# Performance work log

Hardware: AMD Instinct MI355X
Metric: run time of the kernel (lower is better)

Reference implementation:

```python
import jax, jax.numpy as jnp
import numpy as np

ALPHA = 1000.0  # softmin temperature from the original module


def setup_inputs() -> dict:
    key = jax.random.key(0)
    ks = jax.random.split(key, 10)
    B, D, H, E, K = 8192, 784, 256, 32, 512
    s = 0.05  # small init scale to keep activations/distances numerically sane
    return {
        "x": jax.random.normal(ks[0], (B, D), jnp.float32),
        "cluster_reps": jax.random.normal(ks[1], (K, E), jnp.float32),
        "W1": jax.random.normal(ks[2], (D, H), jnp.float32) * s,
        "b1": jnp.zeros((H,), jnp.float32),
        "W2": jax.random.normal(ks[3], (H, E), jnp.float32) * s,
        "b2": jnp.zeros((E,), jnp.float32),
        "W3": jax.random.normal(ks[4], (E, H), jnp.float32) * s,
        "b3": jnp.zeros((H,), jnp.float32),
        "W4": jax.random.normal(ks[5], (H, D), jnp.float32) * s,
        "b4": jnp.zeros((D,), jnp.float32),
    }


def reference(x, cluster_reps, W1, b1, W2, b2, W3, b3, W4, b4):
    # --- autoencoder: 2-layer MLP encoder / decoder ---
    h = jax.nn.relu(x @ W1 + b1)            # [B, H]
    embeddings = h @ W2 + b2                # [B, E]
    h2 = jax.nn.relu(embeddings @ W3 + b3)  # [B, H]
    reconstruction = h2 @ W4 + b4           # [B, D]

    # --- squared distances to cluster reps: [B, K] ---
    diff = embeddings[:, None, :] - cluster_reps[None, :, :]  # [B, K, E]
    distances = jnp.sum(diff * diff, axis=2)                  # [B, K]

    # --- stable softmin-weighted distances ---
    min_dist = jnp.min(distances, axis=1, keepdims=True)       # [B, 1]
    exponentials = jnp.exp(-ALPHA * (distances - min_dist))    # [B, K]
    sum_exponentials = jnp.sum(exponentials, axis=1, keepdims=True)
    weighted_dists = distances * (exponentials / sum_exponentials)

    return (weighted_dists, distances, reconstruction, embeddings)
```

## Files before the change

kernel.cpp:

```cpp
#include <hip/hip_runtime.h>
#include <cstddef>

#define NB 8192
#define ND 784
#define NH 256
#define NE 32
#define NK 512
#define ALPHA_F 1000.0f

typedef _Float16 h8 __attribute__((ext_vector_type(8)));
typedef float f32x4 __attribute__((ext_vector_type(4)));

#define TW1 25
#define TN1 8
#define NBW1 200
#define TW4 8
#define TN4 25
#define NBW4 200
#define NBW2 8
#define NBW3 8

__global__ __launch_bounds__(256)
void prep4_kernel(const float* __restrict__ W1, _Float16* __restrict__ w1thi,
                  _Float16* __restrict__ w1tlo,
                  const float* __restrict__ W4, _Float16* __restrict__ w4thi,
                  _Float16* __restrict__ w4tlo,
                  const float* __restrict__ W2, _Float16* __restrict__ w2thi,
                  _Float16* __restrict__ w2tlo,
                  const float* __restrict__ W3, _Float16* __restrict__ w3thi,
                  _Float16* __restrict__ w3tlo) {
    __shared__ float tile[32][33];
    const int b   = blockIdx.x;
    const int tid = threadIdx.x;

    const float* W; _Float16 *hi, *lo; int K, N, kt, nt;
    if (b < NBW1) {
        W = W1; hi = w1thi; lo = w1tlo; K = ND; N = NH;
        kt = b % TW1; nt = b / TW1;
    } else if (b < NBW1 + NBW4) {
        const int bb = b - NBW1;
        W = W4; hi = w4thi; lo = w4tlo; K = NH; N = ND;
        kt = bb % TW4; nt = bb / TW4;
    } else if (b < NBW1 + NBW4 + NBW2) {
        W = W2; hi = w2thi; lo = w2tlo; K = NH; N = NE;
        kt = b - (NBW1 + NBW4); nt = 0;
    } else {
        W = W3; hi = w3thi; lo = w3tlo; K = NE; N = NH;
        kt = 0; nt = b - (NBW1 + NBW4 + NBW2);
    }
    const int k0 = kt * 32, n0 = nt * 32;
    const int row = tid >> 3, c4 = (tid & 7) * 4;
    #pragma unroll
    for (int j = 0; j < 4; ++j) {
        const int k = k0 + row, n = n0 + c4 + j;
        tile[row][c4 + j] = (k < K && n < N) ? W[(size_t)k * N + n] : 0.f;
    }
    __syncthreads();
    const int n = n0 + row;
    if (n < N) {
        #pragma unroll
        for (int j = 0; j < 4; ++j) {
            const int k = k0 + c4 + j;
            if (k < K) {
                float w = tile[c4 + j][row];
                _Float16 hh = (_Float16)w;
                float r = w - (float)hh;
                hi[(size_t)n * K + k] = hh;
                lo[(size_t)n * K + k] = (_Float16)(r * 2048.0f);
            }
        }
    }
}

__global__ __launch_bounds__(1024, 4)
void mega_kernel(const float* __restrict__ x, const float* __restrict__ reps,
                 const _Float16* __restrict__ w1thi, const _Float16* __restrict__ w1tlo,
                 const _Float16* __restrict__ w2thi, const _Float16* __restrict__ w2tlo,
                 const _Float16* __restrict__ w3thi, const _Float16* __restrict__ w3tlo,
                 const _Float16* __restrict__ w4thi, const _Float16* __restrict__ w4tlo,
                 const float* __restrict__ b1, const float* __restrict__ b2,
                 const float* __restrict__ b3, const float* __restrict__ b4,
                 float* __restrict__ emb_g, float* __restrict__ recon_g,
                 float* __restrict__ dist_g, float* __restrict__ wout_g) {
    __shared__ __align__(16) unsigned char lds[116480];
    _Float16* R0h  = (_Float16*)lds;
    _Float16* sA   = (_Float16*)(lds + 66560);
    _Float16* hP   = (_Float16*)(lds + 74752);
    float*    es   = (float*)(lds + 107520);
    _Float16* eP   = (_Float16*)(lds + 112128);
    float*    rmin = (float*)(lds + 116224);
    float*    rinv = (float*)(lds + 116352);

    const int tid  = threadIdx.x;
    const int lane = tid & 63;
    const int wv   = tid >> 6;
    const int li   = lane & 15;
    const int kq   = (lane >> 4) * 8;
    const int quad = lane >> 4;
    const int r0   = blockIdx.x * 32;

    const float c1 = 1.0f / 2048.0f;
    const float c2 = c1 * c1;

    {
        _Float16* sBhi = R0h;
        _Float16* sBlo = R0h + 2 * 8192;
        _Float16* sAhi = sA;
        _Float16* sAlo = sA + 2 * 1024;
        const int aro  = tid >> 2;
        const int ak   = (tid & 3) * 8;
        const int brow = tid >> 2;
        const int bk   = (tid & 3) * 8;
        const float*    pA  = x + (size_t)(r0 + aro) * ND;
        const _Float16* pBh = w1thi + (size_t)brow * ND;
        const _Float16* pBl = w1tlo + (size_t)brow * ND;

        float araw[8];
        h8 rbh, rbl;

        auto pf = [&](int s) {
            if (tid < 128) {
                const int k = s * 32 + ak;
                if (k + 8 <= ND) {
                    f32x4 v0 = *(const f32x4*)(pA + k);
                    f32x4 v1 = *(const f32x4*)(pA + k + 4);
                    #pragma unroll
                    for (int j = 0; j < 4; ++j) {
                        araw[j] = v0[j]; araw[4 + j] = v1[j];
                    }
                } else {
                    #pragma unroll
                    for (int j = 0; j < 8; ++j) araw[j] = 0.f;
                }
            }
            const int kb = s * 32 + bk;
            rbh = (kb + 8 <= ND) ? *(const h8*)(pBh + kb) : (h8){};
            rbl = (kb + 8 <= ND) ? *(const h8*)(pBl + kb) : (h8){};
        };
        auto cm = [&](int buf) {
            if (tid < 128) {
                h8 hi, lo;
                #pragma unroll
                for (int j = 0; j < 8; ++j) {
                    float v = araw[j];
                    _Float16 hh = (_Float16)v;
                    hi[j] = hh;
                    lo[j] = (_Float16)((v - (float)hh) * 2048.0f);
                }
                *(h8*)&sAhi[buf * 1024 + aro * 32 + ak] = hi;
                *(h8*)&sAlo[buf * 1024 + aro * 32 + ak] = lo;
            }
            *(h8*)&sBhi[buf * 8192 + brow * 32 + bk] = rbh;
            *(h8*)&sBlo[buf * 8192 + brow * 32 + bk] = rbl;
        };

        pf(0); cm(0); pf(1);
        __syncthreads();

        f32x4 a0[2] = {}, a1[2] = {}, a2[2] = {};
        for (int s = 0; s < 25; ++s) {
            const int buf = s & 1;
            h8 fah[2], fal[2];
            #pragma unroll
            for (int mt = 0; mt < 2; ++mt) {
                const int ao = buf * 1024 + (mt * 16 + li) * 32 + kq;
                fah[mt] = *(const h8*)&sAhi[ao];
                fal[mt] = *(const h8*)&sAlo[ao];
            }
            const int bo = buf * 8192 + (wv * 16 + li) * 32 + kq;
            h8 fbh = *(const h8*)&sBhi[bo];
            h8 fbl = *(const h8*)&sBlo[bo];
            #pragma unroll
            for (int mt = 0; mt < 2; ++mt) {
                a0[mt] = __builtin_amdgcn_mfma_f32_16x16x32_f16(fah[mt], fbh, a0[mt], 0, 0, 0);
                a1[mt] = __builtin_amdgcn_mfma_f32_16x16x32_f16(fah[mt], fbl, a1[mt], 0, 0, 0);
                a1[mt] = __builtin_amdgcn_mfma_f32_16x16x32_f16(fal[mt], fbh, a1[mt], 0, 0, 0);
                a2[mt] = __builtin_amdgcn_mfma_f32_16x16x32_f16(fal[mt], fbl, a2[mt], 0, 0, 0);
            }
            if (s + 1 < 25) { cm((s + 1) & 1); if (s + 2 < 25) pf(s + 2); }
            __syncthreads();
        }
        _Float16* hhi = hP;
        _Float16* hlo = hP + 8192;
        const int n  = wv * 16 + li;
        const int nb = n >> 5, nr = n & 31;
        const float bv = b1[n];
        #pragma unroll
        for (int mt = 0; mt < 2; ++mt)
            #pragma unroll
            for (int r = 0; r < 4; ++r) {
                const int m = mt * 16 + quad * 4 + r;
                float v = a0[mt][r] + c1 * a1[mt][r] + c2 * a2[mt][r] + bv;
                v = fmaxf(v, 0.f);
                _Float16 t = (_Float16)v;
                hhi[nb * 1024 + m * 32 + nr] = t;
                hlo[nb * 1024 + m * 32 + nr] = (_Float16)((v - (float)t) * 2048.0f);
            }
    }
    __syncthreads();

    {
        _Float16* w2h = R0h;
        _Float16* w2l = R0h + 8192;
        const int col = tid >> 5;
        const int k8  = tid & 31;
        const int src = col * 256 + k8 * 8;
        const int dst = (k8 >> 2) * 1024 + col * 32 + (k8 & 3) * 8;
        *(h8*)&w2h[dst] = *(const h8*)(w2thi + src);
        *(h8*)&w2l[dst] = *(const h8*)(w2tlo + src);
    }
    __syncthreads();
    if (wv < 4) {
        const int mt = wv >> 1, nt = wv & 1;
        _Float16* hhi = hP;
        _Float16* hlo = hP + 8192;
        _Float16* w2h = R0h;
        _Float16* w2l = R0h + 8192;
        f32x4 e0 = {}, e1 = {}, e2 = {};
        #pragma unroll
        for (int ks = 0; ks < 8; ++ks) {
            h8 ah = *(const h8*)&hhi[ks * 1024 + (mt * 16 + li) * 32 + kq];
            h8 al = *(const h8*)&hlo[ks * 1024 + (mt * 16 + li) * 32 + kq];
            h8 bh = *(const h8*)&w2h[ks * 1024 + (nt * 16 + li) * 32 + kq];
            h8 bl = *(const h8*)&w2l[ks * 1024 + (nt * 16 + li) * 32 + kq];
            e0 = __builtin_amdgcn_mfma_f32_16x16x32_f16(ah, bh, e0, 0, 0, 0);
            e1 = __builtin_amdgcn_mfma_f32_16x16x32_f16(ah, bl, e1, 0, 0, 0);
            e1 = __builtin_amdgcn_mfma_f32_16x16x32_f16(al, bh, e1, 0, 0, 0);
            e2 = __builtin_amdgcn_mfma_f32_16x16x32_f16(al, bl, e2, 0, 0, 0);
        }
        const int col = nt * 16 + li;
        const float bv = b2[col];
        _Float16* eh = eP;
        _Float16* el = eP + 1024;
        #pragma unroll
        for (int r = 0; r < 4; ++r) {
            const int m = mt * 16 + quad * 4 + r;
            float v = e0[r] + c1 * e1[r] + c2 * e2[r] + bv;
            es[m * 36 + col] = v;
            _Float16 t = (_Float16)v;
            eh[m * 32 + col] = t;
            el[m * 32 + col] = (_Float16)((v - (float)t) * 2048.0f);
            emb_g[(size_t)(r0 + m) * NE + col] = v;
        }
    }
    __syncthreads();

    {
        _Float16* w3h = R0h;
        const int o = tid * 8;
        *(h8*)&w3h[o] = *(const h8*)(w3thi + o);
    }
    __syncthreads();
    {
        _Float16* w3h  = R0h;
        _Float16* h2h  = hP;
        _Float16* eh   = eP;
        h8 ah[2];
        #pragma unroll
        for (int mt = 0; mt < 2; ++mt)
            ah[mt] = *(const h8*)&eh[(mt * 16 + li) * 32 + kq];
        const int col = wv * 16 + li;
        h8 bh = *(const h8*)&w3h[col * 32 + kq];
        const float bv = b3[col];
        const int cb = col >> 5, cr = col & 31;
        #pragma unroll
        for (int mt = 0; mt < 2; ++mt) {
            f32x4 q0 = {};
            q0 = __builtin_amdgcn_mfma_f32_16x16x32_f16(ah[mt], bh, q0, 0, 0, 0);
            #pragma unroll
            for (int r = 0; r < 4; ++r) {
                const int m = mt * 16 + quad * 4 + r;
                float v = q0[r] + bv;
                v = fmaxf(v, 0.f);
                h2h[cb * 1024 + m * 32 + cr] = (_Float16)v;
            }
        }
    }
    __syncthreads();

    {
        _Float16* sBhi = R0h;
        _Float16* h2h  = hP;
        const int mt  = wv >> 3;
        const int ntw = wv & 7;
        const int brow = tid >> 2;
        const int bk4  = (tid & 3) * 8;
        h8 rbh[4];
        auto pf = [&](int ss) {
            if (tid < 512 && ss < 56) {
                int rg = (ss >> 3) * 128 + brow;
                if (rg > ND - 1) rg = ND - 1;
                const int k = (ss & 7) * 32 + bk4;
                rbh[ss & 3] = *(const h8*)(w4thi + (size_t)rg * NH + k);
            }
        };
        auto cm = [&](int ss) {
            if (tid < 512 && ss < 56) {
                const int sl = ss & 7;
                *(h8*)&sBhi[sl * 4096 + brow * 32 + bk4] = rbh[ss & 3];
            }
        };
        pf(0); pf(1); pf(2); pf(3);
        cm(0); cm(1); cm(2); cm(3);
        pf(4); pf(5); pf(6); pf(7);
        __syncthreads();

        f32x4 q0 = {};
        auto step = [&](int t) {
            const int sl = t & 7, ks = t & 7;
            const int bo = sl * 4096 + (ntw * 16 + li) * 32 + kq;
            h8 fbh = *(const h8*)&sBhi[bo];
            const int ao = ks * 1024 + (mt * 16 + li) * 32 + kq;
            h8 ah = *(const h8*)&h2h[ao];
            q0 = __builtin_amdgcn_mfma_f32_16x16x32_f16(ah, fbh, q0, 0, 0, 0);
            if (ks == 7) {
                const int n = (t >> 3) * 128 + ntw * 16 + li;
                if (n < ND) {
                    const float bv = b4[n];
                    #pragma unroll
                    for (int r = 0; r < 4; ++r) {
                        const int m = mt * 16 + quad * 4 + r;
                        recon_g[(size_t)(r0 + m) * ND + n] = q0[r] + bv;
                    }
                }
                q0 = {};
            }
        };
        for (int ii = 0; ii < 14; ++ii) {
            const int s0 = ii * 4;
            step(s0); step(s0 + 1); step(s0 + 2); step(s0 + 3);
            cm(s0 + 4); cm(s0 + 5); cm(s0 + 6); cm(s0 + 7);
            pf(s0 + 8); pf(s0 + 9); pf(s0 + 10); pf(s0 + 11);
            __syncthreads();
        }
    }
    __syncthreads();

    {
        float* tr0 = (float*)lds;
        float* tr1 = (float*)(lds + 33280);
        const int half = tid >> 9;
        const int cl   = tid & 511;
        float* trh = half ? tr1 : tr0;
        const int rbase = half * 16;

        const float* rp = reps + (size_t)cl * NE;
        f32x4 rv[8];
        #pragma unroll
        for (int e4 = 0; e4 < 8; ++e4) rv[e4] = ((const f32x4*)rp)[e4];

        float d[16];
        #pragma unroll
        for (int r = 0; r < 16; ++r) {
            float a = 0.f;
            #pragma unroll
            for (int e4 = 0; e4 < 8; ++e4) {
                f32x4 ev = *(const f32x4*)&es[(rbase + r) * 36 + e4 * 4];
                #pragma unroll
                for (int j = 0; j < 4; ++j) {
                    float t = ev[j] - rv[e4][j];
                    a = fmaf(t, t, a);
                }
            }
            d[r] = a;
            trh[r * 520 + cl] = a;
            dist_g[(size_t)(r0 + rbase + r) * NK + cl] = a;
        }
        __syncthreads();
        {
            const int w8 = wv & 7;
            #pragma unroll
            for (int p = 0; p < 2; ++p) {
                const int rl = w8 * 2 + p;
                float m = trh[rl * 520 + lane];
                #pragma unroll
                for (int j = 1; j < 8; ++j)
                    m = fminf(m, trh[rl * 520 + lane + 64 * j]);
                #pragma unroll
                for (int off = 32; off > 0; off >>= 1)
                    m = fminf(m, __shfl_xor(m, off, 64));
                if (lane == 0) rmin[rbase + rl] = m;
            }
        }
        __syncthreads();
        #pragma unroll
        for (int r = 0; r < 16; ++r)
            trh[r * 520 + cl] = expf(-ALPHA_F * (d[r] - rmin[rbase + r]));
        __syncthreads();
        {
            const int w8 = wv & 7;
            #pragma unroll
            for (int p = 0; p < 2; ++p) {
                const int rl = w8 * 2 + p;
                float s = trh[rl * 520 + lane];
                #pragma unroll
                for (int j = 1; j < 8; ++j)
                    s += trh[rl * 520 + lane + 64 * j];
                #pragma unroll
                for (int off = 32; off > 0; off >>= 1)
                    s += __shfl_xor(s, off, 64);
                if (lane == 0) rinv[rbase + rl] = 1.0f / s;
            }
        }
        __syncthreads();
        #pragma unroll
        for (int r = 0; r < 16; ++r) {
            const size_t row = (size_t)(r0 + rbase + r);
            const float ev = trh[r * 520 + cl];
            wout_g[row * NK + cl] = d[r] * (ev * rinv[rbase + r]);
        }
    }
}

__global__ __launch_bounds__(256)
void splitw2_kernel(const float* __restrict__ W1, _Float16* __restrict__ w1thi,
                    _Float16* __restrict__ w1tlo,
                    const float* __restrict__ W4, _Float16* __restrict__ w4thi,
                    _Float16* __restrict__ w4tlo) {
    const int b = blockIdx.x;
    const float* W; _Float16 *hi, *lo; int K, N, n;
    if (b < NH) { W = W1; hi = w1thi; lo = w1tlo; K = ND; N = NH; n = b; }
    else        { W = W4; hi = w4thi; lo = w4tlo; K = NH; N = ND; n = b - NH; }
    for (int k = threadIdx.x; k < K; k += 256) {
        float w = W[(size_t)k * N + n];
        _Float16 hh = (_Float16)w;
        float r = w - (float)hh;
        hi[(size_t)n * K + k] = hh;
        lo[(size_t)n * K + k] = (_Float16)(r * 2048.0f);
    }
}

template<int TERMS, bool RELU, bool SPLITA, int MT>
__global__ __launch_bounds__(256)
void mfma_gemm3(const float* __restrict__ Af32,
                const _Float16* __restrict__ Ahi_g,
                const _Float16* __restrict__ Alo_g,
                const _Float16* __restrict__ WThi,
                const _Float16* __restrict__ WTlo,
                const float* __restrict__ bias, float* __restrict__ C,
                int N, int K, int KS) {
    constexpr int BM  = MT * 32;
    constexpr int ACH = BM / 64;
    constexpr int AS  = BM * 40;
    constexpr int BS  = 64 * 40;
    __shared__ __align__(16) _Float16 smem[2 * BM * 40 * 2 + 2 * 64 * 40 * 2];
    _Float16* sAhi = smem;
    _Float16* sAlo = sAhi + 2 * BM * 40;
    _Float16* sBhi = sAlo + 2 * BM * 40;
    _Float16* sBlo = sBhi + 2 * 64 * 40;

    const int tid = threadIdx.x;
    const int bm  = blockIdx.x * BM;
    const int bn  = blockIdx.y * 64;

    const int arow = (ACH == 1) ? (tid >> 2) : (tid >> 1);
    const int ak   = (ACH == 1) ? ((tid & 3) * 8) : ((tid & 1) * 16);
    const int brow = tid >> 2;
    const int bk   = (tid & 3) * 8;

    const float*    pA32 = SPLITA ? Af32 + (size_t)(bm + arow) * K : nullptr;
    const _Float16* pAhi = SPLITA ? nullptr : Ahi_g + (size_t)(bm + arow) * K;
    const _Float16* pAlo = SPLITA ? nullptr : Alo_g + (size_t)(bm + arow) * K;
    int brow_g = bn + brow; if (brow_g > N - 1) brow_g = N - 1;
    const _Float16* pBhi = WThi + (size_t)brow_g * K;
    const _Float16* pBlo = WTlo + (size_t)brow_g * K;

    float araw[ACH * 8];
    h8 rahi[ACH], ralo[ACH];
    h8 rbhi, rblo;

    auto prefetch = [&](int s) {
        #pragma unroll
        for (int c = 0; c < ACH; ++c) {
            const int k = s * 32 + ak + c * 8;
            if (SPLITA) {
                if (k + 8 <= K) {
                    f32x4 v0 = *(const f32x4*)(pA32 + k);
                    f32x4 v1 = *(const f32x4*)(pA32 + k + 4);
                    #pragma unroll
                    for (int j = 0; j < 4; ++j) {
                        araw[c * 8 + j]     = v0[j];
                        araw[c * 8 + 4 + j] = v1[j];
                    }
                } else {
                    #pragma unroll
                    for (int j = 0; j < 8; ++j) araw[c * 8 + j] = 0.f;
                }
            } else {
                rahi[c] = (k + 8 <= K) ? *(const h8*)(pAhi + k) : (h8){};
                ralo[c] = (k + 8 <= K) ? *(const h8*)(pAlo + k) : (h8){};
            }
        }
        const int kb = s * 32 + bk;
        rbhi = (kb + 8 <= K) ? *(const h8*)(pBhi + kb) : (h8){};
        rblo = (kb + 8 <= K) ? *(const h8*)(pBlo + kb) : (h8){};
    };

    auto commit = [&](int buf) {
        #pragma unroll
        for (int c = 0; c < ACH; ++c) {
            h8 hi, lo;
            if (SPLITA) {
                #pragma unroll
                for (int j = 0; j < 8; ++j) {
                    float v = araw[c * 8 + j];
                    _Float16 hh = (_Float16)v;
                    hi[j] = hh;
                    lo[j] = (_Float16)((v - (float)hh) * 2048.0f);
                }
            } else { hi = rahi[c]; lo = ralo[c]; }
            *(h8*)&sAhi[buf * AS + arow * 40 + ak + c * 8] = hi;
            *(h8*)&sAlo[buf * AS + arow * 40 + ak + c * 8] = lo;
        }
        *(h8*)&sBhi[buf * BS + brow * 40 + bk] = rbhi;
        *(h8*)&sBlo[buf * BS + brow * 40 + bk] = rblo;
    };

    prefetch(0);
    commit(0);
    prefetch(1);
    __syncthreads();

    const int lane = tid & 63;
    const int wv   = tid >> 6;
    const int wm   = (wv >> 1) * (MT * 16);
    const int wn   = (wv & 1) * 32;
    const int li   = lane & 15;
    const int kq   = (lane >> 4) * 8;

    f32x4 acc0[MT][2] = {};
    f32x4 acc1[MT][2] = {};
    f32x4 acc2[MT][2] = {};

    for (int s = 0; s < KS; ++s) {
        const int buf = s & 1;
        h8 fahi[MT], falo[MT], fbhi[2], fblo[2];
        #pragma unroll
        for (int mt = 0; mt < MT; ++mt) {
            const int ao = buf * AS + (wm + mt * 16 + li) * 40 + kq;
            fahi[mt] = *(const h8*)&sAhi[ao];
            falo[mt] = *(const h8*)&sAlo[ao];
        }
        #pragma unroll
        for (int nt = 0; nt < 2; ++nt) {
            const int bo = buf * BS + (wn + nt * 16 + li) * 40 + kq;
            fbhi[nt] = *(const h8*)&sBhi[bo];
            fblo[nt] = *(const h8*)&sBlo[bo];
        }
        #pragma unroll
        for (int mt = 0; mt < MT; ++mt)
            #pragma unroll
            for (int nt = 0; nt < 2; ++nt) {
                acc0[mt][nt] = __builtin_amdgcn_mfma_f32_16x16x32_f16(
                    fahi[mt], fbhi[nt], acc0[mt][nt], 0, 0, 0);
                acc1[mt][nt] = __builtin_amdgcn_mfma_f32_16x16x32_f16(
                    fahi[mt], fblo[nt], acc1[mt][nt], 0, 0, 0);
                acc1[mt][nt] = __builtin_amdgcn_mfma_f32_16x16x32_f16(
                    falo[mt], fbhi[nt], acc1[mt][nt], 0, 0, 0);
                if (TERMS == 4)
                    acc2[mt][nt] = __builtin_amdgcn_mfma_f32_16x16x32_f16(
                        falo[mt], fblo[nt], acc2[mt][nt], 0, 0, 0);
            }
        if (s + 1 < KS) {
            commit((s + 1) & 1);
            if (s + 2 < KS) prefetch(s + 2);
        }
        __syncthreads();
    }

    const float c1 = 1.0f / 2048.0f;
    const float c2 = c1 * c1;
    const int quad = lane >> 4;
    #pragma unroll
    for (int nt = 0; nt < 2; ++nt) {
        const int n = bn + wn + nt * 16 + li;
        if (n < N) {
            const float bv = bias[n];
            #pragma unroll
            for (int mt = 0; mt < MT; ++mt) {
                #pragma unroll
                for (int r = 0; r < 4; ++r) {
                    const int m = bm + wm + mt * 16 + quad * 4 + r;
                    float v = acc0[mt][nt][r] + c1 * acc1[mt][nt][r];
                    if (TERMS == 4) v += c2 * acc2[mt][nt][r];
                    v += bv;
                    if (RELU) v = fmaxf(v, 0.f);
                    C[(size_t)m * N + n] = v;
                }
            }
        }
    }
}

__global__ __launch_bounds__(256)
void mid_kernel(const float* __restrict__ h, const float* __restrict__ W2,
                const float* __restrict__ b2, const float* __restrict__ W3,
                const float* __restrict__ b3, float* __restrict__ emb,
                _Float16* __restrict__ h2hi, _Float16* __restrict__ h2lo) {
    __shared__ float es[16][32];
    const int tid = threadIdx.x;
    const int r0  = blockIdx.x * 16;

    #pragma unroll
    for (int half = 0; half < 2; ++half) {
        const int o   = tid + half * 256;
        const int row = o >> 5;
        const int col = o & 31;
        const float* hrow = h + (size_t)(r0 + row) * NH;
        float acc0 = 0.f, acc1 = 0.f;
        #pragma unroll 4
        for (int k = 0; k < NH; k += 4) {
            float4 hv = *(const float4*)(hrow + k);
            acc0 = fmaf(hv.x, W2[(k + 0) * NE + col], acc0);
            acc1 = fmaf(hv.y, W2[(k + 1) * NE + col], acc1);
            acc0 = fmaf(hv.z, W2[(k + 2) * NE + col], acc0);
            acc1 = fmaf(hv.w, W2[(k + 3) * NE + col], acc1);
        }
        float v = acc0 + acc1 + b2[col];
        es[row][col] = v;
        emb[(size_t)r0 * NE + o] = v;
    }
    __syncthreads();

    const int col = tid;
    float acc[16];
    #pragma unroll
    for (int r = 0; r < 16; ++r) acc[r] = 0.f;
    #pragma unroll
    for (int k = 0; k < NE; ++k) {
        float w = W3[k * NH + col];
        #pragma unroll
        for (int r = 0; r < 16; ++r) acc[r] = fmaf(es[r][k], w, acc[r]);
    }
    const float bb = b3[col];
    #pragma unroll
    for (int r = 0; r < 16; ++r) {
        float v = acc[r] + bb;
        v = v > 0.f ? v : 0.f;
        _Float16 hh = (_Float16)v;
        float rr = v - (float)hh;
        h2hi[(size_t)(r0 + r) * NH + col] = hh;
        h2lo[(size_t)(r0 + r) * NH + col] = (_Float16)(rr * 2048.0f);
    }
}

__global__ __launch_bounds__(512, 4)
void dist_kernel(const float* __restrict__ emb, const float* __restrict__ reps,
                 float* __restrict__ dist, float* __restrict__ wout) {
    __shared__ float es[8][32];
    __shared__ float tr[8][520];
    __shared__ float rmin[8];
    __shared__ float rinv[8];

    const int tid = threadIdx.x;
    const int r0  = blockIdx.x * 8;

    if (tid < 256) es[tid >> 5][tid & 31] = emb[(size_t)r0 * NE + tid];

    const float* rp = reps + (size_t)tid * NE;
    f32x4 rv[8];
    #pragma unroll
    for (int e4 = 0; e4 < 8; ++e4) rv[e4] = ((const f32x4*)rp)[e4];
    __syncthreads();

    float d[8];
    #pragma unroll
    for (int r = 0; r < 8; ++r) {
        float a = 0.f;
        #pragma unroll
        for (int e4 = 0; e4 < 8; ++e4) {
            f32x4 ev = *(const f32x4*)&es[r][e4 * 4];
            #pragma unroll
            for (int j = 0; j < 4; ++j) {
                float t = ev[j] - rv[e4][j];
                a = fmaf(t, t, a);
            }
        }
        d[r] = a;
    }

    const int lane = tid & 63;
    const int wv   = tid >> 6;

    #pragma unroll
    for (int r = 0; r < 8; ++r) tr[r][tid] = d[r];
    __syncthreads();
    {
        f32x4 a = *(const f32x4*)&tr[wv][lane * 8];
        f32x4 b = *(const f32x4*)&tr[wv][lane * 8 + 4];
        float m = fminf(fminf(fminf(a[0], a[1]), fminf(a[2], a[3])),
                        fminf(fminf(b[0], b[1]), fminf(b[2], b[3])));
        #pragma unroll
        for (int off = 32; off > 0; off >>= 1)
            m = fminf(m, __shfl_xor(m, off, 64));
        if (lane == 0) rmin[wv] = m;
    }
    __syncthreads();

    float e[8];
    #pragma unroll
    for (int r = 0; r < 8; ++r) {
        e[r] = expf(-ALPHA_F * (d[r] - rmin[r]));
        tr[r][tid] = e[r];
    }
    __syncthreads();
    {
        f32x4 a = *(const f32x4*)&tr[wv][lane * 8];
        f32x4 b = *(const f32x4*)&tr[wv][lane * 8 + 4];
        float s = ((a[0] + a[1]) + (a[2] + a[3])) +
                  ((b[0] + b[1]) + (b[2] + b[3]));
        #pragma unroll
        for (int off = 32; off > 0; off >>= 1)
            s += __shfl_xor(s, off, 64);
        if (lane == 0) rinv[wv] = 1.0f / s;
    }
    __syncthreads();

    #pragma unroll
    for (int r = 0; r < 8; ++r) {
        const size_t row = (size_t)(r0 + r);
        dist[row * NK + tid] = d[r];
        wout[row * NK + tid] = d[r] * (e[r] * rinv[r]);
    }
}

extern "C" void kernel_launch(void* const* d_in, const int* in_sizes, int n_in,
                              void* d_out, int out_size, void* d_ws, size_t ws_size,
                              hipStream_t stream) {
    const float* x    = (const float*)d_in[0];
    const float* reps = (const float*)d_in[1];
    const float* W1   = (const float*)d_in[2];
    const float* b1   = (const float*)d_in[3];
    const float* W2   = (const float*)d_in[4];
    const float* b2   = (const float*)d_in[5];
    const float* W3   = (const float*)d_in[6];
    const float* b3   = (const float*)d_in[7];
    const float* W4   = (const float*)d_in[8];
    const float* b4   = (const float*)d_in[9];

    float* out   = (float*)d_out;
    float* wout  = out;
    float* dist  = out + (size_t)NB * NK;
    float* recon = out + (size_t)2 * NB * NK;
    float* emb   = out + (size_t)2 * NB * NK + (size_t)NB * ND;

    const size_t nW14 = (size_t)ND * NH;
    const size_t nW23 = (size_t)NE * NH;
    const size_t wneed = (4 * nW14 + 4 * nW23) * sizeof(_Float16);

    if (d_ws != nullptr && ws_size >= wneed) {
        _Float16* w1thi = (_Float16*)d_ws;
        _Float16* w1tlo = w1thi + nW14;
        _Float16* w4thi = w1tlo + nW14;
        _Float16* w4tlo = w4thi + nW14;
        _Float16* w2thi = w4tlo + nW14;
        _Float16* w2tlo = w2thi + nW23;
        _Float16* w3thi = w2tlo + nW23;
        _Float16* w3tlo = w3thi + nW23;

        prep4_kernel<<<NBW1 + NBW4 + NBW2 + NBW3, 256, 0, stream>>>(
            W1, w1thi, w1tlo, W4, w4thi, w4tlo,
            W2, w2thi, w2tlo, W3, w3thi, w3tlo);

        mega_kernel<<<NB / 32, 1024, 0, stream>>>(
            x, reps, w1thi, w1tlo, w2thi, w2tlo, w3thi, w3tlo, w4thi, w4tlo,
            b1, b2, b3, b4, emb, recon, dist, wout);
    } else {
        float* h = dist;
        _Float16* h2hi  = (_Float16*)(dist + (size_t)NB * NH);
        _Float16* h2lo  = h2hi + (size_t)NB * NH;
        _Float16* w1thi = (_Float16*)wout;
        _Float16* w1tlo = w1thi + (size_t)NH * ND;
        _Float16* w4thi = w1tlo + (size_t)NH * ND;
        _Float16* w4tlo = w4thi + (size_t)ND * NH;

        splitw2_kernel<<<NH + ND, 256, 0, stream>>>(W1, w1thi, w1tlo,
                                                    W4, w4thi, w4tlo);
        mfma_gemm3<4, true, true, 2><<<dim3(128, 4), 256, 0, stream>>>(
            x, nullptr, nullptr, w1thi, w1tlo, b1, h, NH, ND, 25);
        mid_kernel<<<NB / 16, 256, 0, stream>>>(h, W2, b2, W3, b3,
                                                emb, h2hi, h2lo);
        mfma_gemm3<3, false, false, 4><<<dim3(64, 13), 256, 0, stream>>>(
            nullptr, h2hi, h2lo, w4thi, w4tlo, b4, recon, ND, NH, 8);
        dist_kernel<<<NB / 8, 512, 0, stream>>>(emb, reps, dist, wout);
    }
}
```

Before: 146.2 us.

## Load W4 fragments directly from global into registers, dropping LDS staging

The decoder output GEMM no longer stages W4 tiles through shared memory with per-step barriers. Each wave loads its B fragments straight from global memory into a double-buffered register array and prefetches the next 128-column panel while the current one runs through MFMAs. This removes the LDS writes and reads and the 14 block-wide syncs. In exchange it raises register pressure, and W4 is now fetched redundantly by the two waves that share an ntw, since each wave loads its own copy.

```diff
diff --git a/kernel.cpp b/kernel.cpp
--- a/kernel.cpp
+++ b/kernel.cpp
@@ -279,62 +279,38 @@
     __syncthreads();
 
     {
-        _Float16* sBhi = R0h;
-        _Float16* h2h  = hP;
+        _Float16* h2h = hP;
         const int mt  = wv >> 3;
         const int ntw = wv & 7;
-        const int brow = tid >> 2;
-        const int bk4  = (tid & 3) * 8;
-        h8 rbh[4];
-        auto pf = [&](int ss) {
-            if (tid < 512 && ss < 56) {
-                int rg = (ss >> 3) * 128 + brow;
-                if (rg > ND - 1) rg = ND - 1;
-                const int k = (ss & 7) * 32 + bk4;
-                rbh[ss & 3] = *(const h8*)(w4thi + (size_t)rg * NH + k);
-            }
+        h8 rb[2][8];
+        auto ldp = [&](int p, int sl) {
+            int n = p * 128 + ntw * 16 + li;
+            if (n > ND - 1) n = ND - 1;
+            const _Float16* pb = w4thi + (size_t)n * NH;
+            #pragma unroll
+            for (int ks = 0; ks < 8; ++ks)
+                rb[sl][ks] = *(const h8*)(pb + ks * 32 + kq);
         };
-        auto cm = [&](int ss) {
-            if (tid < 512 && ss < 56) {
-                const int sl = ss & 7;
-                *(h8*)&sBhi[sl * 4096 + brow * 32 + bk4] = rbh[ss & 3];
-            }
-        };
-        pf(0); pf(1); pf(2); pf(3);
-        cm(0); cm(1); cm(2); cm(3);
-        pf(4); pf(5); pf(6); pf(7);
-        __syncthreads();
-
-        f32x4 q0 = {};
-        auto step = [&](int t) {
-            const int sl = t & 7, ks = t & 7;
-            const int bo = sl * 4096 + (ntw * 16 + li) * 32 + kq;
-            h8 fbh = *(const h8*)&sBhi[bo];
-            const int ao = ks * 1024 + (mt * 16 + li) * 32 + kq;
-            h8 ah = *(const h8*)&h2h[ao];
-            q0 = __builtin_amdgcn_mfma_f32_16x16x32_f16(ah, fbh, q0, 0, 0, 0);
-            if (ks == 7) {
-                const int n = (t >> 3) * 128 + ntw * 16 + li;
-                if (n < ND) {
-                    const float bv = b4[n];
-                    #pragma unroll
-                    for (int r = 0; r < 4; ++r) {
-                        const int m = mt * 16 + quad * 4 + r;
-                        recon_g[(size_t)(r0 + m) * ND + n] = q0[r] + bv;
-                    }
-                }
-                q0 = {};
-            }
-        };
-        for (int ii = 0; ii < 14; ++ii) {
-            const int s0 = ii * 4;
-            step(s0); step(s0 + 1); step(s0 + 2); step(s0 + 3);
-            cm(s0 + 4); cm(s0 + 5); cm(s0 + 6); cm(s0 + 7);
-            pf(s0 + 8); pf(s0 + 9); pf(s0 + 10); pf(s0 + 11);
-            __syncthreads();
-        }
-    }
-    __syncthreads();
+        ldp(0, 0);
+        #pragma unroll
+        for (int p = 0; p < 7; ++p) {
+            const int cur = p & 1;
+            if (p + 1 < 7) ldp(p + 1, cur ^ 1);
+            f32x4 q0 = {};
+            #pragma unroll
+            for (int ks = 0; ks < 8; ++ks) {
+                h8 ah = *(const h8*)&h2h[ks * 1024 + (mt * 16 + li) * 32 + kq];
+                q0 = __builtin_amdgcn_mfma_f32_16x16x32_f16(ah, rb[cur][ks], q0, 0, 0, 0);
+            }
+            const int n = p * 128 + ntw * 16 + li;
+            if (n < ND) {
+                const float bv = b4[n];
+                #pragma unroll
+                for (int r = 0; r < 4; ++r)
+                    recon_g[(size_t)(r0 + mt * 16 + quad * 4 + r) * ND + n] = q0[r] + bv;
+            }
+        }
+    }
 
     {
         float* tr0 = (float*)lds;
```

After: 158.5 us. 8.4% more time.
